# Kernel optimization log

Measured on AMD Instinct MI355X. Metric: run time of the kernel, lower is better.

The kernel has to match this reference:

```python
import jax, jax.numpy as jnp
import numpy as np

V, P = 50000, 50
WE, PE = 300, 100
LH = 800            # bidirectional total hidden
H = LH // 2         # per-direction hidden = 400
MH = 1024           # mlp_hidden_dim
B, T = 32, 128


def setup_inputs() -> dict:
    key = jax.random.key(0)
    ks = jax.random.split(key, 16)
    s = 0.05
    inp = {
        "word_tensor": jax.random.randint(ks[0], (B, T), 0, V, dtype=jnp.int32),
        "word_lengths": jnp.full((B,), T, dtype=jnp.int32),
        "pos_tensor": jax.random.randint(ks[1], (B, T), 0, P, dtype=jnp.int32),
        "word_emb": jax.random.normal(ks[2], (V, WE), jnp.float32) * s,
        "pos_emb": jax.random.normal(ks[3], (P, PE), jnp.float32) * s,
        # LSTM layer 0: input dim WE+PE=400; stacked over 2 directions
        "Wih0": jax.random.normal(ks[4], (2, 4 * H, WE + PE), jnp.float32) * s,
        "Whh0": jax.random.normal(ks[5], (2, 4 * H, H), jnp.float32) * s,
        "b0": jnp.zeros((2, 4 * H), jnp.float32),
        # LSTM layer 1: input dim = 2*H = 800
        "Wih1": jax.random.normal(ks[6], (2, 4 * H, LH), jnp.float32) * s,
        "Whh1": jax.random.normal(ks[7], (2, 4 * H, H), jnp.float32) * s,
        "b1": jnp.zeros((2, 4 * H), jnp.float32),
        "Wh": jax.random.normal(ks[8], (MH // 2, LH), jnp.float32) * s,
        "bh": jnp.zeros((MH // 2,), jnp.float32),
        "Wm": jax.random.normal(ks[9], (MH // 2, LH), jnp.float32) * s,
        "bm": jnp.zeros((MH // 2,), jnp.float32),
        "Wo": jax.random.normal(ks[10], (1, MH), jnp.float32) * s,
        "bo": jnp.zeros((1,), jnp.float32),
    }
    return inp


def _lstm_dir(x_tbd, W_ih, W_hh, bias, reverse):
    # x_tbd: [T,B,D]; PyTorch gate order i,f,g,o
    Bsz = x_tbd.shape[1]
    Hd = W_hh.shape[1]
    def cell(carry, xt):
        h, c = carry
        g = xt @ W_ih.T + h @ W_hh.T + bias
        i, f, gg, o = jnp.split(g, 4, axis=-1)
        c = jax.nn.sigmoid(f) * c + jax.nn.sigmoid(i) * jnp.tanh(gg)
        h = jax.nn.sigmoid(o) * jnp.tanh(c)
        return (h, c), h
    init = (jnp.zeros((Bsz, Hd), x_tbd.dtype), jnp.zeros((Bsz, Hd), x_tbd.dtype))
    _, hs = jax.lax.scan(cell, init, x_tbd, reverse=reverse)
    return hs  # [T,B,H], in original time order


def _bilstm_layer(x_btd, Wih, Whh, b):
    x_tbd = jnp.swapaxes(x_btd, 0, 1)
    fwd = _lstm_dir(x_tbd, Wih[0], Whh[0], b[0], reverse=False)
    bwd = _lstm_dir(x_tbd, Wih[1], Whh[1], b[1], reverse=True)
    out = jnp.concatenate([fwd, bwd], axis=-1)  # [T,B,2H]
    return jnp.swapaxes(out, 0, 1)              # [B,T,2H]


def reference(word_tensor, word_lengths, pos_tensor, word_emb, pos_emb,
              Wih0, Whh0, b0, Wih1, Whh1, b1,
              Wh, bh, Wm, bm, Wo, bo):
    embeds = jnp.concatenate([word_emb[word_tensor], pos_emb[pos_tensor]], axis=2)  # [B,T,400]
    h1 = _bilstm_layer(embeds, Wih0, Whh0, b0)   # [B,T,800]
    lstm_out = _bilstm_layer(h1, Wih1, Whh1, b1)  # [B,T,800]
    head_f = lstm_out @ Wh.T + bh   # [B,T,512]
    modif_f = lstm_out @ Wm.T + bm  # [B,T,512]
    # score[b,h,m] = Wo @ tanh(cat(head_f[b,h], modif_f[b,m])) + bo
    # tanh(cat(a,b)) = cat(tanh(a), tanh(b)) -> exact decomposition
    half = Wo.shape[1] // 2
    s_h = jnp.tanh(head_f) @ Wo[0, :half]   # [B,T]
    s_m = jnp.tanh(modif_f) @ Wo[0, half:]  # [B,T]
    score = s_h[:, :, None] + s_m[:, None, :] + bo[0]  # [B,T,T]
    return score
```

## Files before the change

### kernel.cpp

```cpp
#include <hip/hip_runtime.h>

#define DEV __device__ __forceinline__

typedef _Float16 f16;
typedef _Float16 f16x8 __attribute__((ext_vector_type(8)));
typedef float f32x4 __attribute__((ext_vector_type(4)));
typedef unsigned long long ull;

static constexpr int K0P  = 416;
static constexpr int NBLK = 13;
static constexpr int GN   = 3328;
static constexpr int WKP  = 424;
static constexpr int HX_OFF = 128 * WKP * 2;
static constexpr int FL_OFF = HX_OFF + 13 * 2560;
static constexpr int SMEM_LSTM = FL_OFF + 16;
static constexpr int HB1_ELEM  = 2 * 128 * 13 * 1024;
static constexpr int HB_BYTES  = 2 * HB1_ELEM * 2;
static constexpr unsigned READY0 = 0x80008000u;

DEV float sigf(float x) { return 1.f / (1.f + __expf(-x)); }
DEV float tanhf_(float x) {
  x = fminf(10.f, fmaxf(-10.f, x));
  float e = __expf(2.f * x);
  return (e - 1.f) / (e + 1.f);
}
DEV ull  AL8(const ull* p) { return __hip_atomic_load(p, __ATOMIC_RELAXED, __HIP_MEMORY_SCOPE_AGENT); }
DEV void AS4(unsigned* p, unsigned v) { __hip_atomic_store(p, v, __ATOMIC_RELAXED, __HIP_MEMORY_SCOPE_AGENT); }


__global__ void embed_k(const int* __restrict__ wt, const int* __restrict__ pt,
                        const float* __restrict__ we, const float* __restrict__ pe,
                        f16* __restrict__ x0)
{
  const int r = blockIdx.x;
  const int tid = threadIdx.x;
  const int w = wt[r], p = pt[r];
  const float* wrow = we + (size_t)w * 300;
  const float* prow = pe + (size_t)p * 100;
  f16* xr = x0 + (size_t)r * K0P;
  for (int k = tid; k < K0P; k += 128) {
    float v = (k < 300) ? wrow[k] : (k < 400 ? prow[k - 300] : 0.f);
    xr[k] = (f16)v;
  }
}

__global__ void convpad_k(const float* __restrict__ src, f16* __restrict__ dst,
                          int rows, int K, int KP)
{
  const size_t total = (size_t)rows * KP;
  for (size_t i = (size_t)blockIdx.x * blockDim.x + threadIdx.x; i < total;
       i += (size_t)gridDim.x * blockDim.x) {
    int r = (int)(i / KP), k = (int)(i % KP);
    dst[i] = (f16)(k < K ? src[(size_t)r * K + k] : 0.f);
  }
}

__global__ void wih_reorder_k(const float* __restrict__ src, const float* __restrict__ bias,
                              f16* __restrict__ dst, float* __restrict__ biasr,
                              int K, int KP)
{
  const size_t total = (size_t)GN * KP;
  for (size_t i = (size_t)blockIdx.x * blockDim.x + threadIdx.x; i < total;
       i += (size_t)gridDim.x * blockDim.x) {
    int k = (int)(i % KP);
    int R = (int)(i / KP);
    int d = R / 1664, rr = R % 1664, blk = rr >> 7, loc = rr & 127;
    int w = loc >> 5, t = (loc >> 4) & 1, fq = (loc >> 2) & 3, g = loc & 3;
    int u = blk * 32 + w * 8 + 2 * fq + t;
    float v = (u < 400 && k < K) ? src[((size_t)d * 1600 + g * 400 + u) * K + k] : 0.f;
    dst[i] = (f16)v;
    if (k == 0) biasr[R] = (u < 400) ? bias[d * 1600 + g * 400 + u] : 0.f;
  }
}

__global__ void whh_reorder_k(const float* __restrict__ src, f16* __restrict__ dst)
{
  const int total = 2 * NBLK * 128 * WKP;
  for (int i = blockIdx.x * blockDim.x + threadIdx.x; i < total;
       i += gridDim.x * blockDim.x) {
    int k = i % WKP, loc = (i / WKP) & 127, blk = (i / (WKP * 128)) % NBLK,
        d = i / (WKP * 128 * NBLK);
    int w = loc >> 5, t = (loc >> 4) & 1, fq = (loc >> 2) & 3, g = loc & 3;
    int u = blk * 32 + w * 8 + 2 * fq + t;
    float v = (u < 400 && k < 400) ? src[((size_t)d * 1600 + g * 400 + u) * 400 + k] : 0.f;
    dst[i] = (f16)v;
  }
}

__global__ void biascat_k(const float* __restrict__ bh, const float* __restrict__ bm,
                          float* __restrict__ bhm)
{
  int i = threadIdx.x;
  bhm[i] = i < 512 ? bh[i] : bm[i - 512];
}

__global__ void init_hb_k(unsigned* __restrict__ p, int n)
{
  for (int i = blockIdx.x * blockDim.x + threadIdx.x; i < n; i += gridDim.x * blockDim.x) {
    int off = i % (13 * 512);
    int blk = off >> 9, win = off & 511;
    bool pad = (blk == 12) && ((win >> 7) & 1);
    p[i] = pad ? READY0 : 0u;
  }
}

__global__ __launch_bounds__(256) void gemm_f16_nt(
    const f16* __restrict__ A, const f16* __restrict__ Bw,
    const float* __restrict__ bias, float* __restrict__ C,
    int M, int N, int KP)
{
  __shared__ __align__(16) f16 As[128][40];
  __shared__ __align__(16) f16 Bs[128][40];
  const int tid = threadIdx.x;
  const int bn = blockIdx.x, bm = blockIdx.y;
  const int lane = tid & 63, wid = tid >> 6;
  const int wr = wid >> 1, wc = wid & 1;
  const int srow = tid >> 1, shalf = tid & 1;
  const f16* Ap = A + (size_t)(bm * 128 + srow) * KP + shalf * 16;
  const f16* Bp = Bw + (size_t)(bn * 128 + srow) * KP + shalf * 16;
  const int fr = lane & 15, fq = lane >> 4;
  f32x4 acc[4][4] = {};
  for (int kt = 0; kt < KP; kt += 32) {
    __syncthreads();
    *(uint4*)&As[srow][shalf * 16]     = *(const uint4*)(Ap + kt);
    *(uint4*)&As[srow][shalf * 16 + 8] = *(const uint4*)(Ap + kt + 8);
    *(uint4*)&Bs[srow][shalf * 16]     = *(const uint4*)(Bp + kt);
    *(uint4*)&Bs[srow][shalf * 16 + 8] = *(const uint4*)(Bp + kt + 8);
    __syncthreads();
    f16x8 af[4], bf[4];
    #pragma unroll
    for (int m = 0; m < 4; ++m) af[m] = *(const f16x8*)&As[wr * 64 + m * 16 + fr][fq * 8];
    #pragma unroll
    for (int n = 0; n < 4; ++n) bf[n] = *(const f16x8*)&Bs[wc * 64 + n * 16 + fr][fq * 8];
    #pragma unroll
    for (int m = 0; m < 4; ++m)
      #pragma unroll
      for (int n = 0; n < 4; ++n)
        acc[m][n] = __builtin_amdgcn_mfma_f32_16x16x32_f16(af[m], bf[n], acc[m][n], 0, 0, 0);
  }
  #pragma unroll
  for (int n = 0; n < 4; ++n) {
    const int gn = bn * 128 + wc * 64 + n * 16 + fr;
    const float bv = bias ? bias[gn] : 0.f;
    #pragma unroll
    for (int m = 0; m < 4; ++m) {
      const size_t gm = (size_t)bm * 128 + wr * 64 + m * 16 + fq * 4;
      #pragma unroll
      for (int r = 0; r < 4; ++r)
        C[(gm + r) * (size_t)N + gn] = acc[m][n][r] + bv;
    }
  }
}

__global__ __launch_bounds__(256) void lstm_mfma_k(
    const float* __restrict__ gates,
    const f16* __restrict__ whh_r,
    f16* __restrict__ h_out,
    f16* __restrict__ hB)
{
  extern __shared__ __align__(16) char smem[];
  f16*  W_lds = (f16*)smem;
  char* hx    = smem + HX_OFF;
  int*  flags = (int*)(smem + FL_OFF);

  const int d = blockIdx.x / NBLK, blk = blockIdx.x % NBLK;
  const int tid = threadIdx.x;
  const int lane = tid & 63, w = tid >> 6;
  const int fr = lane & 15, fq = lane >> 4;

  {
    const uint4* src = (const uint4*)(whh_r + ((size_t)d * NBLK + blk) * 128 * WKP);
    uint4* dst = (uint4*)W_lds;
    for (int i = tid; i < 128 * WKP / 8; i += 256) dst[i] = src[i];
  }
  if (tid < 2) flags[tid] = 0;
  __syncthreads();

  const int u0 = blk * 32 + w * 8 + 2 * fq;
  const bool ok = u0 < 400;
  const float* gbase0 = gates + (size_t)(fr * 128) * GN + d * 1664 + blk * 128 + w * 32;
  const float* gbase1 = gbase0 + (size_t)16 * 128 * GN;
  f16* hout0 = h_out + (size_t)(fr * 128) * 800 + d * 400;
  f16* hout1 = hout0 + (size_t)16 * 128 * 800;
  const f16* a0base = W_lds + (size_t)(w * 32 + fr) * WKP + fq * 8;
  const f16* a1base = a0base + 16 * WKP;
  f16* hb_d = hB + (size_t)d * 128 * 13 * 1024;

  const int nkk = (w == 0) ? 4 : 3;
  const int kk0 = (w == 0) ? 0 : 4 + 3 * (w - 1);

  float c00 = 0.f, c01 = 0.f, c10 = 0.f, c11 = 0.f;

  for (int s = 0; s < 128; ++s) {
    const int t = d ? 127 - s : s;
    f32x4 acc00 = {}, acc01 = {}, acc10 = {}, acc11 = {};
    float4 p00, p10, p01, p11;

    if (s > 0) {
      const ull* slab = (const ull*)(hb_d + (size_t)(s - 1) * 13 * 1024) + lane * 2;
      ull q[4][4];
      const unsigned full = (1u << nkk) - 1;
      unsigned pend = (nkk == 4) ? 0xFFFFu : 0x0FFFu;
      unsigned wrote = 0, flagged = 0;
      int* fw = &flags[s & 1];
      while (flagged != full) {
        #pragma unroll
        for (int i = 0; i < 4; ++i)
          if (i < nkk) {
            const ull* pp = slab + (kk0 + i) * 256;
            if ((pend >> (i * 4 + 0)) & 1) q[i][0] = AL8(pp);
            if ((pend >> (i * 4 + 1)) & 1) q[i][1] = AL8(pp + 1);
            if ((pend >> (i * 4 + 2)) & 1) q[i][2] = AL8(pp + 128);
            if ((pend >> (i * 4 + 3)) & 1) q[i][3] = AL8(pp + 129);
          }
        __builtin_amdgcn_sched_barrier(0);
        #pragma unroll
        for (int i = 0; i < 4; ++i)
          if (i < nkk)
            #pragma unroll
            for (int j = 0; j < 4; ++j)
              if ((pend >> (i * 4 + j)) & 1) {
                ull v = q[i][j];
                if ((unsigned)v != 0u && (unsigned)(v >> 32) != 0u)
                  pend &= ~(1u << (i * 4 + j));
              }
        #pragma unroll
        for (int i = 0; i < 4; ++i)
          if (i < nkk && !((wrote >> i) & 1) && ((pend >> (i * 4)) & 15u) == 0u) {
            char* hp = hx + (kk0 + i) * 2560 + lane * 40;
            *(ull*)(hp +  0) = q[i][0];
            *(ull*)(hp +  8) = q[i][1];
            *(ull*)(hp + 16) = q[i][2];
            *(ull*)(hp + 24) = q[i][3];
            wrote |= 1u << i;
          }
        #pragma unroll
        for (int i = 0; i < 4; ++i)
          if (i < nkk && !((flagged >> i) & 1)) {
            bool done = ((pend >> (i * 4)) & 15u) == 0u;
            if (__all(done)) {
              asm volatile("s_waitcnt lgkmcnt(0)" ::: "memory");
              if (lane == 0)
                __hip_atomic_fetch_or(fw, 1 << (kk0 + i), __ATOMIC_RELAXED,
                                      __HIP_MEMORY_SCOPE_WORKGROUP);
              flagged |= 1u << i;
            }
          }
        if (flagged != full) __builtin_amdgcn_s_sleep(2);
      }
      const float* g0 = gbase0 + (size_t)t * GN;
      const float* g1 = gbase1 + (size_t)t * GN;
      p00 = *(const float4*)(g0 + fq * 4);
      p10 = *(const float4*)(g0 + 16 + fq * 4);
      p01 = *(const float4*)(g1 + fq * 4);
      p11 = *(const float4*)(g1 + 16 + fq * 4);
      while ((__hip_atomic_load(fw, __ATOMIC_ACQUIRE, __HIP_MEMORY_SCOPE_WORKGROUP)
              & 0x1FFF) != 0x1FFF)
        __builtin_amdgcn_s_sleep(1);
      __builtin_amdgcn_sched_barrier(0);
      #pragma unroll
      for (int kk = 0; kk < 13; ++kk) {
        const char* hp = hx + kk * 2560 + lane * 40;
        f16x8 a0 = *(const f16x8*)(a0base + kk * 32);
        f16x8 a1 = *(const f16x8*)(a1base + kk * 32);
        union { ull u[2]; f16x8 v; } B0, B1;
        B0.u[0] = *(const ull*)(hp);      B0.u[1] = *(const ull*)(hp + 8);
        B1.u[0] = *(const ull*)(hp + 16); B1.u[1] = *(const ull*)(hp + 24);
        acc00 = __builtin_amdgcn_mfma_f32_16x16x32_f16(a0, B0.v, acc00, 0, 0, 0);
        acc01 = __builtin_amdgcn_mfma_f32_16x16x32_f16(a0, B1.v, acc01, 0, 0, 0);
        acc10 = __builtin_amdgcn_mfma_f32_16x16x32_f16(a1, B0.v, acc10, 0, 0, 0);
        acc11 = __builtin_amdgcn_mfma_f32_16x16x32_f16(a1, B1.v, acc11, 0, 0, 0);
      }
    } else {
      const float* g0 = gbase0 + (size_t)t * GN;
      const float* g1 = gbase1 + (size_t)t * GN;
      p00 = *(const float4*)(g0 + fq * 4);
      p10 = *(const float4*)(g0 + 16 + fq * 4);
      p01 = *(const float4*)(g1 + fq * 4);
      p11 = *(const float4*)(g1 + 16 + fq * 4);
    }

    __syncthreads();
    if (tid == 0)
      __hip_atomic_store(&flags[s & 1], 0, __ATOMIC_RELAXED, __HIP_MEMORY_SCOPE_WORKGROUP);

    auto act = [&](const f32x4& a, const float4& p, float& c) -> f16 {
      float vi = a[0] + p.x, vf = a[1] + p.y, vg = a[2] + p.z, vo = a[3] + p.w;
      c = sigf(vf) * c + sigf(vi) * tanhf_(vg);
      return (f16)(sigf(vo) * tanhf_(c));
    };
    f16 h00 = act(acc00, p00, c00);
    f16 h10 = act(acc10, p10, c10);
    f16 h01 = act(acc01, p01, c01);
    f16 h11 = act(acc11, p11, c11);

    if (ok) {
      unsigned pk0 = (unsigned)__builtin_bit_cast(unsigned short, h00) |
                     ((unsigned)__builtin_bit_cast(unsigned short, h10) << 16);
      unsigned pk1 = (unsigned)__builtin_bit_cast(unsigned short, h01) |
                     ((unsigned)__builtin_bit_cast(unsigned short, h11) << 16);
      if (pk0 == 0u) pk0 = READY0;
      if (pk1 == 0u) pk1 = READY0;
      unsigned* hbw = (unsigned*)(hb_d + (size_t)s * 13 * 1024 + blk * 1024
                                  + (w * 16 + fr) * 8) + fq;
      AS4(hbw, pk0);
      AS4(hbw + 256, pk1);
      *(unsigned*)(hout0 + (size_t)t * 800 + u0) = pk0;
      *(unsigned*)(hout1 + (size_t)t * 800 + u0) = pk1;
    }
  }
}

__global__ __launch_bounds__(256) void tail_k(const float* __restrict__ feat,
                                              const float* __restrict__ wo,
                                              float* __restrict__ s_h,
                                              float* __restrict__ s_m)
{
  const int r = blockIdx.x;
  const int tid = threadIdx.x;
  const float* fr = feat + (size_t)r * 1024;
  float sum = 0.f;
  const int n0 = tid * 4;
  #pragma unroll
  for (int j = 0; j < 4; ++j) sum += tanhf_(fr[n0 + j]) * wo[n0 + j];
  #pragma unroll
  for (int off = 32; off > 0; off >>= 1) sum += __shfl_down(sum, off, 64);
  __shared__ float red[4];
  if ((tid & 63) == 0) red[tid >> 6] = sum;
  __syncthreads();
  if (tid == 0)       s_h[r] = red[0] + red[1];
  else if (tid == 64) s_m[r] = red[2] + red[3];
}

__global__ void score_k(const float* __restrict__ s_h, const float* __restrict__ s_m,
                        const float* __restrict__ bo, float* __restrict__ out)
{
  const int bh = blockIdx.x;
  const int m = threadIdx.x;
  out[(size_t)bh * 128 + m] = s_h[bh] + s_m[(bh & ~127) + m] + bo[0];
}

extern "C" void kernel_launch(void* const* d_in, const int* in_sizes, int n_in,
                              void* d_out, int out_size, void* d_ws, size_t ws_size,
                              hipStream_t stream)
{
  const int*   wt   = (const int*)d_in[0];
  const int*   pt   = (const int*)d_in[2];
  const float* we   = (const float*)d_in[3];
  const float* pe   = (const float*)d_in[4];
  const float* Wih0 = (const float*)d_in[5];
  const float* Whh0 = (const float*)d_in[6];
  const float* b0   = (const float*)d_in[7];
  const float* Wih1 = (const float*)d_in[8];
  const float* Whh1 = (const float*)d_in[9];
  const float* b1   = (const float*)d_in[10];
  const float* Wh   = (const float*)d_in[11];
  const float* bh   = (const float*)d_in[12];
  const float* Wm   = (const float*)d_in[13];
  const float* bm   = (const float*)d_in[14];
  const float* Wo   = (const float*)d_in[15];
  const float* bo   = (const float*)d_in[16];
  float* out = (float*)d_out;

  char* p = (char*)d_ws;
  auto alloc = [&](size_t bytes) { char* q = p; p += (bytes + 255) & ~(size_t)255; return q; };
  f16*   x0    = (f16*)alloc((size_t)4096 * K0P * 2);
  f16*   wihr0 = (f16*)alloc((size_t)GN * K0P * 2);
  f16*   wihr1 = (f16*)alloc((size_t)GN * 800 * 2);
  f16*   whhr0 = (f16*)alloc((size_t)2 * NBLK * 128 * WKP * 2);
  f16*   whhr1 = (f16*)alloc((size_t)2 * NBLK * 128 * WKP * 2);
  f16*   whm   = (f16*)alloc((size_t)1024 * 800 * 2);
  float* biasr0= (float*)alloc(GN * 4);
  float* biasr1= (float*)alloc(GN * 4);
  float* bhm   = (float*)alloc(1024 * 4);
  float* sh    = (float*)alloc(4096 * 4);
  float* sm    = (float*)alloc(4096 * 4);
  f16*   h1    = (f16*)alloc((size_t)4096 * 800 * 2);
  f16*   h2    = (f16*)alloc((size_t)4096 * 800 * 2);
  f16*   hB    = (f16*)alloc(HB_BYTES);
  float* gates = (float*)alloc((size_t)4096 * GN * 4);
  float* feat  = (float*)gates;

  static bool attr_set = false;
  if (!attr_set) {
    hipFuncSetAttribute((const void*)lstm_mfma_k,
                        hipFuncAttributeMaxDynamicSharedMemorySize, SMEM_LSTM);
    attr_set = true;
  }

  init_hb_k<<<512, 256, 0, stream>>>((unsigned*)hB, HB_BYTES / 4);
  embed_k<<<4096, 128, 0, stream>>>(wt, pt, we, pe, x0);
  wih_reorder_k<<<1024, 256, 0, stream>>>(Wih0, b0, wihr0, biasr0, 400, K0P);
  wih_reorder_k<<<1024, 256, 0, stream>>>(Wih1, b1, wihr1, biasr1, 800, 800);
  whh_reorder_k<<<1024, 256, 0, stream>>>(Whh0, whhr0);
  whh_reorder_k<<<1024, 256, 0, stream>>>(Whh1, whhr1);
  convpad_k<<<1024, 256, 0, stream>>>(Wh, whm, 512, 800, 800);
  convpad_k<<<1024, 256, 0, stream>>>(Wm, whm + (size_t)512 * 800, 512, 800, 800);
  biascat_k<<<1, 1024, 0, stream>>>(bh, bm, bhm);

  gemm_f16_nt<<<dim3(26, 32), 256, 0, stream>>>(x0, wihr0, biasr0, gates, 4096, GN, K0P);
  lstm_mfma_k<<<26, 256, SMEM_LSTM, stream>>>(gates, whhr0, h1, hB);
  gemm_f16_nt<<<dim3(26, 32), 256, 0, stream>>>(h1, wihr1, biasr1, gates, 4096, GN, 800);
  lstm_mfma_k<<<26, 256, SMEM_LSTM, stream>>>(gates, whhr1, h2, hB + HB1_ELEM);
  gemm_f16_nt<<<dim3(8, 32), 256, 0, stream>>>(h2, whm, bhm, feat, 4096, 1024, 800);
  tail_k<<<4096, 256, 0, stream>>>(feat, Wo, sh, sm);
  score_k<<<4096, 128, 0, stream>>>(sh, sm, bo, out);
}
```

Measured before the change: 1.366 ms.

## Co-locate each LSTM direction's blocks on one XCD and use non-atomic polling

The recurrent LSTM kernel now launches 256 blocks. Each block reads its XCC id and claims a role so that the 13 blocks of each direction land on the same XCD; extra blocks exit. A probe checks whether all blocks of a direction can see each other's writes through plain volatile accesses; if so, the step-to-step h exchange uses volatile loads and stores instead of agent-scope atomics. The loop also prefetches the next step's input gates and spins with less sleep, and the h_out writes are moved to a separate unpack kernel. This relies on undocumented XCD placement and L2 coherence behaviour, adds launch and handshake overhead, and falls back to the atomic path when the probe fails.

```diff
diff --git a/kernel.cpp b/kernel.cpp
--- a/kernel.cpp
+++ b/kernel.cpp
@@ -26,6 +26,8 @@
 }
 DEV ull  AL8(const ull* p) { return __hip_atomic_load(p, __ATOMIC_RELAXED, __HIP_MEMORY_SCOPE_AGENT); }
 DEV void AS4(unsigned* p, unsigned v) { __hip_atomic_store(p, v, __ATOMIC_RELAXED, __HIP_MEMORY_SCOPE_AGENT); }
+DEV int  ALi(const int* p) { return __hip_atomic_load(p, __ATOMIC_RELAXED, __HIP_MEMORY_SCOPE_AGENT); }
+DEV void AAi(int* p, int v) { __hip_atomic_fetch_add(p, v, __ATOMIC_RELAXED, __HIP_MEMORY_SCOPE_AGENT); }
 
 
 __global__ void embed_k(const int* __restrict__ wt, const int* __restrict__ pt,
@@ -94,6 +96,12 @@
   bhm[i] = i < 512 ? bh[i] : bm[i - 512];
 }
 
+__global__ void zero_k(int* __restrict__ p, int n)
+{
+  for (int i = blockIdx.x * blockDim.x + threadIdx.x; i < n; i += gridDim.x * blockDim.x)
+    p[i] = 0;
+}
+
 __global__ void init_hb_k(unsigned* __restrict__ p, int n)
 {
   for (int i = blockIdx.x * blockDim.x + threadIdx.x; i < n; i += gridDim.x * blockDim.x) {
@@ -101,6 +109,23 @@
     int blk = off >> 9, win = off & 511;
     bool pad = (blk == 12) && ((win >> 7) & 1);
     p[i] = pad ? READY0 : 0u;
+  }
+}
+
+__global__ __launch_bounds__(256) void unpack_k(const f16* __restrict__ hBl,
+                                                f16* __restrict__ h_out)
+{
+  const int d = blockIdx.x >> 7, s = blockIdx.x & 127;
+  const int t = d ? 127 - s : s;
+  const unsigned* slab = (const unsigned*)(hBl + ((size_t)d * 128 + s) * 13 * 1024);
+  for (int j = threadIdx.x; j < 13 * 512; j += 256) {
+    const int blk = j >> 9, q = j & 511, half = q >> 8, q2 = q & 255;
+    const int fq = q2 & 3, fr = (q2 >> 2) & 15, w = q2 >> 6;
+    const int u0 = blk * 32 + w * 8 + 2 * fq;
+    if (u0 < 400) {
+      const int b = fr + 16 * half;
+      *(unsigned*)(h_out + (size_t)(b * 128 + t) * 800 + d * 400 + u0) = slab[j];
+    }
   }
 }
 
@@ -152,66 +177,46 @@
   }
 }
 
-__global__ __launch_bounds__(256) void lstm_mfma_k(
-    const float* __restrict__ gates,
-    const f16* __restrict__ whh_r,
-    f16* __restrict__ h_out,
-    f16* __restrict__ hB)
-{
-  extern __shared__ __align__(16) char smem[];
-  f16*  W_lds = (f16*)smem;
-  char* hx    = smem + HX_OFF;
-  int*  flags = (int*)(smem + FL_OFF);
-
-  const int d = blockIdx.x / NBLK, blk = blockIdx.x % NBLK;
-  const int tid = threadIdx.x;
-  const int lane = tid & 63, w = tid >> 6;
-  const int fr = lane & 15, fq = lane >> 4;
-
-  {
-    const uint4* src = (const uint4*)(whh_r + ((size_t)d * NBLK + blk) * 128 * WKP);
-    uint4* dst = (uint4*)W_lds;
-    for (int i = tid; i < 128 * WKP / 8; i += 256) dst[i] = src[i];
-  }
-  if (tid < 2) flags[tid] = 0;
-  __syncthreads();
-
-  const int u0 = blk * 32 + w * 8 + 2 * fq;
-  const bool ok = u0 < 400;
-  const float* gbase0 = gates + (size_t)(fr * 128) * GN + d * 1664 + blk * 128 + w * 32;
-  const float* gbase1 = gbase0 + (size_t)16 * 128 * GN;
-  f16* hout0 = h_out + (size_t)(fr * 128) * 800 + d * 400;
-  f16* hout1 = hout0 + (size_t)16 * 128 * 800;
-  const f16* a0base = W_lds + (size_t)(w * 32 + fr) * WKP + fq * 8;
-  const f16* a1base = a0base + 16 * WKP;
-  f16* hb_d = hB + (size_t)d * 128 * 13 * 1024;
-
+template<bool FAST>
+DEV void lstm_loop(const float* gbase0, const float* gbase1,
+                   const f16* a0base, const f16* a1base,
+                   f16* hb_d, char* hx, int* lflag,
+                   int d, int blk, int w, int lane, int fr, int fq, int tid, bool ok)
+{
   const int nkk = (w == 0) ? 4 : 3;
   const int kk0 = (w == 0) ? 0 : 4 + 3 * (w - 1);
-
   float c00 = 0.f, c01 = 0.f, c10 = 0.f, c11 = 0.f;
 
+  float4 pc00, pc10, pc01, pc11;
+  {
+    const int t0 = d ? 127 : 0;
+    const float* g0 = gbase0 + (size_t)t0 * GN;
+    const float* g1 = gbase1 + (size_t)t0 * GN;
+    pc00 = *(const float4*)(g0 + fq * 4);
+    pc10 = *(const float4*)(g0 + 16 + fq * 4);
+    pc01 = *(const float4*)(g1 + fq * 4);
+    pc11 = *(const float4*)(g1 + 16 + fq * 4);
+  }
+
   for (int s = 0; s < 128; ++s) {
-    const int t = d ? 127 - s : s;
     f32x4 acc00 = {}, acc01 = {}, acc10 = {}, acc11 = {};
-    float4 p00, p10, p01, p11;
-
+    int* fw = &lflag[s & 1];
     if (s > 0) {
       const ull* slab = (const ull*)(hb_d + (size_t)(s - 1) * 13 * 1024) + lane * 2;
       ull q[4][4];
       const unsigned full = (1u << nkk) - 1;
       unsigned pend = (nkk == 4) ? 0xFFFFu : 0x0FFFu;
       unsigned wrote = 0, flagged = 0;
-      int* fw = &flags[s & 1];
+      int rnd = 0;
       while (flagged != full) {
         #pragma unroll
         for (int i = 0; i < 4; ++i)
           if (i < nkk) {
             const ull* pp = slab + (kk0 + i) * 256;
-            if ((pend >> (i * 4 + 0)) & 1) q[i][0] = AL8(pp);
-            if ((pend >> (i * 4 + 1)) & 1) q[i][1] = AL8(pp + 1);
-            if ((pend >> (i * 4 + 2)) & 1) q[i][2] = AL8(pp + 128);
-            if ((pend >> (i * 4 + 3)) & 1) q[i][3] = AL8(pp + 129);
+            if ((pend >> (i * 4 + 0)) & 1) q[i][0] = FAST ? *(volatile const ull*)pp        : AL8(pp);
+            if ((pend >> (i * 4 + 1)) & 1) q[i][1] = FAST ? *(volatile const ull*)(pp + 1)  : AL8(pp + 1);
+            if ((pend >> (i * 4 + 2)) & 1) q[i][2] = FAST ? *(volatile const ull*)(pp + 128): AL8(pp + 128);
+            if ((pend >> (i * 4 + 3)) & 1) q[i][3] = FAST ? *(volatile const ull*)(pp + 129): AL8(pp + 129);
           }
         __builtin_amdgcn_sched_barrier(0);
         #pragma unroll
@@ -246,14 +251,22 @@
               flagged |= 1u << i;
             }
           }
-        if (flagged != full) __builtin_amdgcn_s_sleep(2);
+        if (flagged != full && ++rnd >= 2) __builtin_amdgcn_s_sleep(1);
       }
-      const float* g0 = gbase0 + (size_t)t * GN;
-      const float* g1 = gbase1 + (size_t)t * GN;
-      p00 = *(const float4*)(g0 + fq * 4);
-      p10 = *(const float4*)(g0 + 16 + fq * 4);
-      p01 = *(const float4*)(g1 + fq * 4);
-      p11 = *(const float4*)(g1 + 16 + fq * 4);
+    }
+
+    float4 pn00 = pc00, pn10 = pc10, pn01 = pc01, pn11 = pc11;
+    if (s < 127) {
+      const int tn = d ? 126 - s : s + 1;
+      const float* g0 = gbase0 + (size_t)tn * GN;
+      const float* g1 = gbase1 + (size_t)tn * GN;
+      pn00 = *(const float4*)(g0 + fq * 4);
+      pn10 = *(const float4*)(g0 + 16 + fq * 4);
+      pn01 = *(const float4*)(g1 + fq * 4);
+      pn11 = *(const float4*)(g1 + 16 + fq * 4);
+    }
+
+    if (s > 0) {
       while ((__hip_atomic_load(fw, __ATOMIC_ACQUIRE, __HIP_MEMORY_SCOPE_WORKGROUP)
               & 0x1FFF) != 0x1FFF)
         __builtin_amdgcn_s_sleep(1);
@@ -271,28 +284,21 @@
         acc10 = __builtin_amdgcn_mfma_f32_16x16x32_f16(a1, B0.v, acc10, 0, 0, 0);
         acc11 = __builtin_amdgcn_mfma_f32_16x16x32_f16(a1, B1.v, acc11, 0, 0, 0);
       }
-    } else {
-      const float* g0 = gbase0 + (size_t)t * GN;
-      const float* g1 = gbase1 + (size_t)t * GN;
-      p00 = *(const float4*)(g0 + fq * 4);
-      p10 = *(const float4*)(g0 + 16 + fq * 4);
-      p01 = *(const float4*)(g1 + fq * 4);
-      p11 = *(const float4*)(g1 + 16 + fq * 4);
     }
 
     __syncthreads();
     if (tid == 0)
-      __hip_atomic_store(&flags[s & 1], 0, __ATOMIC_RELAXED, __HIP_MEMORY_SCOPE_WORKGROUP);
+      __hip_atomic_store(fw, 0, __ATOMIC_RELAXED, __HIP_MEMORY_SCOPE_WORKGROUP);
 
     auto act = [&](const f32x4& a, const float4& p, float& c) -> f16 {
       float vi = a[0] + p.x, vf = a[1] + p.y, vg = a[2] + p.z, vo = a[3] + p.w;
       c = sigf(vf) * c + sigf(vi) * tanhf_(vg);
       return (f16)(sigf(vo) * tanhf_(c));
     };
-    f16 h00 = act(acc00, p00, c00);
-    f16 h10 = act(acc10, p10, c10);
-    f16 h01 = act(acc01, p01, c01);
-    f16 h11 = act(acc11, p11, c11);
+    f16 h00 = act(acc00, pc00, c00);
+    f16 h10 = act(acc10, pc10, c10);
+    f16 h01 = act(acc01, pc01, c01);
+    f16 h11 = act(acc11, pc11, c11);
 
     if (ok) {
       unsigned pk0 = (unsigned)__builtin_bit_cast(unsigned short, h00) |
@@ -303,12 +309,107 @@
       if (pk1 == 0u) pk1 = READY0;
       unsigned* hbw = (unsigned*)(hb_d + (size_t)s * 13 * 1024 + blk * 1024
                                   + (w * 16 + fr) * 8) + fq;
-      AS4(hbw, pk0);
-      AS4(hbw + 256, pk1);
-      *(unsigned*)(hout0 + (size_t)t * 800 + u0) = pk0;
-      *(unsigned*)(hout1 + (size_t)t * 800 + u0) = pk1;
-    }
-  }
+      if (FAST) {
+        *(volatile unsigned*)hbw = pk0;
+        *(volatile unsigned*)(hbw + 256) = pk1;
+      } else {
+        AS4(hbw, pk0);
+        AS4(hbw + 256, pk1);
+      }
+    }
+    pc00 = pn00; pc10 = pn10; pc01 = pn01; pc11 = pn11;
+  }
+}
+
+__global__ __launch_bounds__(256) void lstm_mfma_k(
+    const float* __restrict__ gates,
+    const f16* __restrict__ whh_r,
+    f16* __restrict__ hB,
+    int* __restrict__ ctrl,
+    ull* __restrict__ prb)
+{
+  extern __shared__ __align__(16) char smem[];
+  f16*  W_lds = (f16*)smem;
+  char* hx    = smem + HX_OFF;
+  int*  lflag = (int*)(smem + FL_OFF);
+  __shared__ int role_sh, fast_sh;
+
+  const int tid = threadIdx.x;
+  const int lane = tid & 63, w = tid >> 6;
+  const int fr = lane & 15, fq = lane >> 4;
+
+  if (tid == 0) {
+    int xcc;
+    asm volatile("s_getreg_b32 %0, hwreg(HW_REG_XCC_ID)" : "=s"(xcc));
+    xcc &= 7;
+    int role = -1;
+    if (xcc < 2) {
+      int r = atomicAdd(&ctrl[xcc], 1);
+      if (r < NBLK) role = xcc * NBLK + r;
+    }
+    AAi(&ctrl[2], 1);
+    if (role < 0) {
+      while (ALi(&ctrl[2]) < (int)gridDim.x) __builtin_amdgcn_s_sleep(8);
+      for (int dd = 0; dd < 2 && role < 0; ++dd) {
+        int r = atomicAdd(&ctrl[dd], 1);
+        if (r < NBLK) role = dd * NBLK + r;
+      }
+    }
+    role_sh = (role < 0) ? -1 : (role | ((xcc == role / NBLK) ? 256 : 0));
+  }
+  __syncthreads();
+  const int rs = role_sh;
+  if (rs < 0) return;
+  const int role = rs & 255;
+  const bool home = (rs & 256) != 0;
+  const int d = role / NBLK, blk = role % NBLK;
+
+  {
+    const uint4* src = (const uint4*)(whh_r + ((size_t)d * NBLK + blk) * 128 * WKP);
+    uint4* dst = (uint4*)W_lds;
+    for (int i = tid; i < 128 * WKP / 8; i += 256) dst[i] = src[i];
+  }
+  if (tid < 2) lflag[tid] = 0;
+  __syncthreads();
+
+  if (w == 0) {
+    volatile ull* pb = (volatile ull*)(prb + (size_t)d * 13 * 8);
+    ull sink = (lane < 13) ? pb[lane * 8] : 0;
+    asm volatile("" :: "v"((unsigned)(sink & 1)));
+    if (lane == 0) {
+      AAi(&ctrl[4 + d], 1);
+      while (ALi(&ctrl[4 + d]) < NBLK) __builtin_amdgcn_s_sleep(2);
+      pb[blk * 8] = 0xDEADBEEFCAFEF00Dull;
+    }
+    int seen = 0;
+    for (int r = 0; r < 2048 && !seen; ++r) {
+      ull v = (lane < 13) ? pb[lane * 8] : 1;
+      seen = (~__ballot(v != 0)) == 0ull ? 1 : 0;
+    }
+    if (lane == 0) {
+      AAi(&ctrl[6 + d], (seen && home) ? 1 : 0);
+      AAi(&ctrl[8 + d], 1);
+      while (ALi(&ctrl[8 + d]) < NBLK) __builtin_amdgcn_s_sleep(2);
+      fast_sh = (ALi(&ctrl[6 + d]) == NBLK) ? 1 : 0;
+    }
+  }
+  __syncthreads();
+  const bool fast = fast_sh != 0;
+
+  const int u0 = blk * 32 + w * 8 + 2 * fq;
+  const bool ok = u0 < 400;
+  const float* gbase0 = gates + (size_t)(fr * 128) * GN + d * 1664 + blk * 128 + w * 32;
+  const float* gbase1 = gbase0 + (size_t)16 * 128 * GN;
+  const f16* a0base = W_lds + (size_t)(w * 32 + fr) * WKP + fq * 8;
+  const f16* a1base = a0base + 16 * WKP;
+  f16* hb_d = hB + (size_t)d * 128 * 13 * 1024;
+
+  if (fast)
+    lstm_loop<true >(gbase0, gbase1, a0base, a1base, hb_d, hx, lflag,
+                     d, blk, w, lane, fr, fq, tid, ok);
+  else
+    lstm_loop<false>(gbase0, gbase1, a0base, a1base, hb_d, hx, lflag,
+                     d, blk, w, lane, fr, fq, tid, ok);
 }
 
 __global__ __launch_bounds__(256) void tail_k(const float* __restrict__ feat,
@@ -378,6 +479,8 @@
   f16*   h1    = (f16*)alloc((size_t)4096 * 800 * 2);
   f16*   h2    = (f16*)alloc((size_t)4096 * 800 * 2);
   f16*   hB    = (f16*)alloc(HB_BYTES);
+  int*   ctrl  = (int*)alloc(2 * 16 * 4);
+  ull*   prb   = (ull*)alloc(2 * 208 * 8);
   float* gates = (float*)alloc((size_t)4096 * GN * 4);
   float* feat  = (float*)gates;
 
@@ -389,6 +492,8 @@
   }
 
   init_hb_k<<<512, 256, 0, stream>>>((unsigned*)hB, HB_BYTES / 4);
+  zero_k<<<1, 256, 0, stream>>>(ctrl, 32);
+  zero_k<<<2, 256, 0, stream>>>((int*)prb, 832);
   embed_k<<<4096, 128, 0, stream>>>(wt, pt, we, pe, x0);
   wih_reorder_k<<<1024, 256, 0, stream>>>(Wih0, b0, wihr0, biasr0, 400, K0P);
   wih_reorder_k<<<1024, 256, 0, stream>>>(Wih1, b1, wihr1, biasr1, 800, 800);
@@ -399,9 +504,12 @@
   biascat_k<<<1, 1024, 0, stream>>>(bh, bm, bhm);
 
   gemm_f16_nt<<<dim3(26, 32), 256, 0, stream>>>(x0, wihr0, biasr0, gates, 4096, GN, K0P);
-  lstm_mfma_k<<<26, 256, SMEM_LSTM, stream>>>(gates, whhr0, h1, hB);
+  lstm_mfma_k<<<256, 256, SMEM_LSTM, stream>>>(gates, whhr0, hB, ctrl, prb);
+  unpack_k<<<256, 256, 0, stream>>>(hB, h1);
   gemm_f16_nt<<<dim3(26, 32), 256, 0, stream>>>(h1, wihr1, biasr1, gates, 4096, GN, 800);
-  lstm_mfma_k<<<26, 256, SMEM_LSTM, stream>>>(gates, whhr1, h2, hB + HB1_ELEM);
+  lstm_mfma_k<<<256, 256, SMEM_LSTM, stream>>>(gates, whhr1, hB + HB1_ELEM,
+                                               ctrl + 16, prb + 208);
+  unpack_k<<<256, 256, 0, stream>>>(hB + HB1_ELEM, h2);
   gemm_f16_nt<<<dim3(8, 32), 256, 0, stream>>>(h2, whm, bhm, feat, 4096, 1024, 800);
   tail_k<<<4096, 256, 0, stream>>>(feat, Wo, sh, sm);
   score_k<<<4096, 128, 0, stream>>>(sh, sm, bo, out);
```

Measured after the change: 1.795 ms. 1.31x slower.

## Keep W_hh in registers and overlap recurrent MFMA with per-slice h arrival

Applied to the files above, without the earlier changes.

The recurrent LSTM kernel now holds its W_hh slice in VGPRs instead of LDS. It double-buffers the staged hidden state and replaces the single bitmask barrier with per-slice step counters, so each wave runs MFMAs on K-slices as soon as they arrive rather than waiting for all 13. Gate preactivations for the next step are prefetched, and the strided h_out stores are removed from the serial loop, with a separate unpack kernel scattering the hB buffer into the layer output afterwards. The aim is to shorten the per-timestep critical path in the latency-bound recurrence, at the cost of heavy register pressure (104 extra VGPRs for weights) and two extra kernel launches.

```diff
diff --git a/kernel.cpp b/kernel.cpp
--- a/kernel.cpp
+++ b/kernel.cpp
@@ -11,9 +11,8 @@
 static constexpr int NBLK = 13;
 static constexpr int GN   = 3328;
 static constexpr int WKP  = 424;
-static constexpr int HX_OFF = 128 * WKP * 2;
-static constexpr int FL_OFF = HX_OFF + 13 * 2560;
-static constexpr int SMEM_LSTM = FL_OFF + 16;
+static constexpr int HXP  = 13 * 2560;
+static constexpr int SMEM_LSTM = 2 * HXP + 64;
 static constexpr int HB1_ELEM  = 2 * 128 * 13 * 1024;
 static constexpr int HB_BYTES  = 2 * HB1_ELEM * 2;
 static constexpr unsigned READY0 = 0x80008000u;
@@ -100,7 +99,24 @@
     int off = i % (13 * 512);
     int blk = off >> 9, win = off & 511;
     bool pad = (blk == 12) && ((win >> 7) & 1);
-    p[i] = pad ? READY0 : 0u;
+    AS4(p + i, pad ? READY0 : 0u);
+  }
+}
+
+__global__ __launch_bounds__(256) void unpack_k(const f16* __restrict__ hBl,
+                                                f16* __restrict__ h_out)
+{
+  const int d = blockIdx.x >> 7, s = blockIdx.x & 127;
+  const int t = d ? 127 - s : s;
+  const unsigned* slab = (const unsigned*)(hBl + ((size_t)d * 128 + s) * 13 * 1024);
+  for (int j = threadIdx.x; j < 13 * 512; j += 256) {
+    const int blk = j >> 9, q = j & 511, half = q >> 8, q2 = q & 255;
+    const int fq = q2 & 3, fr = (q2 >> 2) & 15, w = q2 >> 6;
+    const int u0 = blk * 32 + w * 8 + 2 * fq;
+    if (u0 < 400) {
+      const int b = fr + 16 * half;
+      *(unsigned*)(h_out + (size_t)(b * 128 + t) * 800 + d * 400 + u0) = slab[j];
+    }
   }
 }
 
@@ -152,147 +168,155 @@
   }
 }
 
-__global__ __launch_bounds__(256) void lstm_mfma_k(
+__global__ __launch_bounds__(256, 1) void lstm_mfma_k(
     const float* __restrict__ gates,
     const f16* __restrict__ whh_r,
-    f16* __restrict__ h_out,
     f16* __restrict__ hB)
 {
   extern __shared__ __align__(16) char smem[];
-  f16*  W_lds = (f16*)smem;
-  char* hx    = smem + HX_OFF;
-  int*  flags = (int*)(smem + FL_OFF);
+  char* hx   = smem;
+  int*  flds = (int*)(smem + 2 * HXP);
 
   const int d = blockIdx.x / NBLK, blk = blockIdx.x % NBLK;
   const int tid = threadIdx.x;
   const int lane = tid & 63, w = tid >> 6;
   const int fr = lane & 15, fq = lane >> 4;
 
-  {
-    const uint4* src = (const uint4*)(whh_r + ((size_t)d * NBLK + blk) * 128 * WKP);
-    uint4* dst = (uint4*)W_lds;
-    for (int i = tid; i < 128 * WKP / 8; i += 256) dst[i] = src[i];
-  }
-  if (tid < 2) flags[tid] = 0;
-  __syncthreads();
+  if (tid < 13) flds[tid] = -1;
+
+  const f16* wr0 = whh_r + ((size_t)(d * NBLK + blk) * 128 + w * 32 + fr) * WKP + fq * 8;
+  const f16* wr1 = wr0 + (size_t)16 * WKP;
+  f16x8 a0r[13], a1r[13];
+  #pragma unroll
+  for (int kk = 0; kk < 13; ++kk) {
+    a0r[kk] = *(const f16x8*)(wr0 + kk * 32);
+    a1r[kk] = *(const f16x8*)(wr1 + kk * 32);
+  }
 
   const int u0 = blk * 32 + w * 8 + 2 * fq;
   const bool ok = u0 < 400;
   const float* gbase0 = gates + (size_t)(fr * 128) * GN + d * 1664 + blk * 128 + w * 32;
   const float* gbase1 = gbase0 + (size_t)16 * 128 * GN;
-  f16* hout0 = h_out + (size_t)(fr * 128) * 800 + d * 400;
-  f16* hout1 = hout0 + (size_t)16 * 128 * 800;
-  const f16* a0base = W_lds + (size_t)(w * 32 + fr) * WKP + fq * 8;
-  const f16* a1base = a0base + 16 * WKP;
   f16* hb_d = hB + (size_t)d * 128 * 13 * 1024;
-
   const int nkk = (w == 0) ? 4 : 3;
   const int kk0 = (w == 0) ? 0 : 4 + 3 * (w - 1);
+  const unsigned ownfull = (1u << nkk) - 1;
 
   float c00 = 0.f, c01 = 0.f, c10 = 0.f, c11 = 0.f;
+  float4 pc00, pc10, pc01, pc11;
+  {
+    const int t0 = d ? 127 : 0;
+    const float* g0 = gbase0 + (size_t)t0 * GN;
+    const float* g1 = gbase1 + (size_t)t0 * GN;
+    pc00 = *(const float4*)(g0 + fq * 4);
+    pc10 = *(const float4*)(g0 + 16 + fq * 4);
+    pc01 = *(const float4*)(g1 + fq * 4);
+    pc11 = *(const float4*)(g1 + 16 + fq * 4);
+  }
+  __syncthreads();
 
   for (int s = 0; s < 128; ++s) {
-    const int t = d ? 127 - s : s;
     f32x4 acc00 = {}, acc01 = {}, acc10 = {}, acc11 = {};
-    float4 p00, p10, p01, p11;
-
     if (s > 0) {
       const ull* slab = (const ull*)(hb_d + (size_t)(s - 1) * 13 * 1024) + lane * 2;
+      char* hxw = hx + (s & 1) * HXP;
       ull q[4][4];
-      const unsigned full = (1u << nkk) - 1;
       unsigned pend = (nkk == 4) ? 0xFFFFu : 0x0FFFu;
-      unsigned wrote = 0, flagged = 0;
-      int* fw = &flags[s & 1];
-      while (flagged != full) {
-        #pragma unroll
-        for (int i = 0; i < 4; ++i)
-          if (i < nkk) {
-            const ull* pp = slab + (kk0 + i) * 256;
-            if ((pend >> (i * 4 + 0)) & 1) q[i][0] = AL8(pp);
-            if ((pend >> (i * 4 + 1)) & 1) q[i][1] = AL8(pp + 1);
-            if ((pend >> (i * 4 + 2)) & 1) q[i][2] = AL8(pp + 128);
-            if ((pend >> (i * 4 + 3)) & 1) q[i][3] = AL8(pp + 129);
+      unsigned stagedm = 0;
+      unsigned flagged = 0;
+      unsigned done = 0;
+      while (done != 0x1FFFu) {
+        bool progress = false;
+        if (flagged != ownfull) {
+          #pragma unroll
+          for (int i = 0; i < 4; ++i)
+            if (i < nkk && !((flagged >> i) & 1)) {
+              const ull* pp = slab + (kk0 + i) * 256;
+              if ((pend >> (i * 4 + 0)) & 1) q[i][0] = AL8(pp);
+              if ((pend >> (i * 4 + 1)) & 1) q[i][1] = AL8(pp + 1);
+              if ((pend >> (i * 4 + 2)) & 1) q[i][2] = AL8(pp + 128);
+              if ((pend >> (i * 4 + 3)) & 1) q[i][3] = AL8(pp + 129);
+            }
+          __builtin_amdgcn_sched_barrier(0);
+          #pragma unroll
+          for (int i = 0; i < 4; ++i)
+            if (i < nkk && !((flagged >> i) & 1)) {
+              #pragma unroll
+              for (int j = 0; j < 4; ++j)
+                if ((pend >> (i * 4 + j)) & 1) {
+                  ull v = q[i][j];
+                  if ((unsigned)v != 0u && (unsigned)(v >> 32) != 0u)
+                    pend &= ~(1u << (i * 4 + j));
+                }
+              if (!((stagedm >> i) & 1) && ((pend >> (i * 4)) & 15u) == 0u) {
+                char* hp = hxw + (kk0 + i) * 2560 + lane * 40;
+                *(ull*)(hp +  0) = q[i][0];
+                *(ull*)(hp +  8) = q[i][1];
+                *(ull*)(hp + 16) = q[i][2];
+                *(ull*)(hp + 24) = q[i][3];
+                stagedm |= 1u << i;
+              }
+              bool dn = (stagedm >> i) & 1;
+              if (__all(dn)) {
+                asm volatile("s_waitcnt lgkmcnt(0)" ::: "memory");
+                if (lane == 0)
+                  __hip_atomic_store(&flds[kk0 + i], s, __ATOMIC_RELAXED,
+                                     __HIP_MEMORY_SCOPE_WORKGROUP);
+                flagged |= 1u << i;
+                progress = true;
+              }
+            }
+        }
+        {
+          int fv = (lane < 13)
+                     ? __hip_atomic_load(&flds[lane], __ATOMIC_RELAXED,
+                                         __HIP_MEMORY_SCOPE_WORKGROUP)
+                     : 0x7fffffff;
+          unsigned rdy = (unsigned)__ballot(fv >= s) & 0x1FFFu;
+          unsigned todo = rdy & ~done;
+          if (todo) {
+            progress = true;
+            #pragma unroll
+            for (int kk = 0; kk < 13; ++kk)
+              if ((todo >> kk) & 1) {
+                const char* hp = hxw + kk * 2560 + lane * 40;
+                union { ull u[2]; f16x8 v; } B0, B1;
+                B0.u[0] = *(const ull*)(hp);      B0.u[1] = *(const ull*)(hp + 8);
+                B1.u[0] = *(const ull*)(hp + 16); B1.u[1] = *(const ull*)(hp + 24);
+                acc00 = __builtin_amdgcn_mfma_f32_16x16x32_f16(a0r[kk], B0.v, acc00, 0, 0, 0);
+                acc01 = __builtin_amdgcn_mfma_f32_16x16x32_f16(a0r[kk], B1.v, acc01, 0, 0, 0);
+                acc10 = __builtin_amdgcn_mfma_f32_16x16x32_f16(a1r[kk], B0.v, acc10, 0, 0, 0);
+                acc11 = __builtin_amdgcn_mfma_f32_16x16x32_f16(a1r[kk], B1.v, acc11, 0, 0, 0);
+              }
+            done |= todo;
           }
-        __builtin_amdgcn_sched_barrier(0);
-        #pragma unroll
-        for (int i = 0; i < 4; ++i)
-          if (i < nkk)
-            #pragma unroll
-            for (int j = 0; j < 4; ++j)
-              if ((pend >> (i * 4 + j)) & 1) {
-                ull v = q[i][j];
-                if ((unsigned)v != 0u && (unsigned)(v >> 32) != 0u)
-                  pend &= ~(1u << (i * 4 + j));
-              }
-        #pragma unroll
-        for (int i = 0; i < 4; ++i)
-          if (i < nkk && !((wrote >> i) & 1) && ((pend >> (i * 4)) & 15u) == 0u) {
-            char* hp = hx + (kk0 + i) * 2560 + lane * 40;
-            *(ull*)(hp +  0) = q[i][0];
-            *(ull*)(hp +  8) = q[i][1];
-            *(ull*)(hp + 16) = q[i][2];
-            *(ull*)(hp + 24) = q[i][3];
-            wrote |= 1u << i;
-          }
-        #pragma unroll
-        for (int i = 0; i < 4; ++i)
-          if (i < nkk && !((flagged >> i) & 1)) {
-            bool done = ((pend >> (i * 4)) & 15u) == 0u;
-            if (__all(done)) {
-              asm volatile("s_waitcnt lgkmcnt(0)" ::: "memory");
-              if (lane == 0)
-                __hip_atomic_fetch_or(fw, 1 << (kk0 + i), __ATOMIC_RELAXED,
-                                      __HIP_MEMORY_SCOPE_WORKGROUP);
-              flagged |= 1u << i;
-            }
-          }
-        if (flagged != full) __builtin_amdgcn_s_sleep(2);
+        }
+        if (!progress && done != 0x1FFFu) __builtin_amdgcn_s_sleep(1);
       }
-      const float* g0 = gbase0 + (size_t)t * GN;
-      const float* g1 = gbase1 + (size_t)t * GN;
-      p00 = *(const float4*)(g0 + fq * 4);
-      p10 = *(const float4*)(g0 + 16 + fq * 4);
-      p01 = *(const float4*)(g1 + fq * 4);
-      p11 = *(const float4*)(g1 + 16 + fq * 4);
-      while ((__hip_atomic_load(fw, __ATOMIC_ACQUIRE, __HIP_MEMORY_SCOPE_WORKGROUP)
-              & 0x1FFF) != 0x1FFF)
-        __builtin_amdgcn_s_sleep(1);
-      __builtin_amdgcn_sched_barrier(0);
-      #pragma unroll
-      for (int kk = 0; kk < 13; ++kk) {
-        const char* hp = hx + kk * 2560 + lane * 40;
-        f16x8 a0 = *(const f16x8*)(a0base + kk * 32);
-        f16x8 a1 = *(const f16x8*)(a1base + kk * 32);
-        union { ull u[2]; f16x8 v; } B0, B1;
-        B0.u[0] = *(const ull*)(hp);      B0.u[1] = *(const ull*)(hp + 8);
-        B1.u[0] = *(const ull*)(hp + 16); B1.u[1] = *(const ull*)(hp + 24);
-        acc00 = __builtin_amdgcn_mfma_f32_16x16x32_f16(a0, B0.v, acc00, 0, 0, 0);
-        acc01 = __builtin_amdgcn_mfma_f32_16x16x32_f16(a0, B1.v, acc01, 0, 0, 0);
-        acc10 = __builtin_amdgcn_mfma_f32_16x16x32_f16(a1, B0.v, acc10, 0, 0, 0);
-        acc11 = __builtin_amdgcn_mfma_f32_16x16x32_f16(a1, B1.v, acc11, 0, 0, 0);
-      }
-    } else {
-      const float* g0 = gbase0 + (size_t)t * GN;
-      const float* g1 = gbase1 + (size_t)t * GN;
-      p00 = *(const float4*)(g0 + fq * 4);
-      p10 = *(const float4*)(g0 + 16 + fq * 4);
-      p01 = *(const float4*)(g1 + fq * 4);
-      p11 = *(const float4*)(g1 + 16 + fq * 4);
     }
 
+    float4 pn00 = pc00, pn10 = pc10, pn01 = pc01, pn11 = pc11;
+    if (s < 127) {
+      const int tn = d ? 126 - s : s + 1;
+      const float* g0 = gbase0 + (size_t)tn * GN;
+      const float* g1 = gbase1 + (size_t)tn * GN;
+      pn00 = *(const float4*)(g0 + fq * 4);
+      pn10 = *(const float4*)(g0 + 16 + fq * 4);
+      pn01 = *(const float4*)(g1 + fq * 4);
+      pn11 = *(const float4*)(g1 + 16 + fq * 4);
+    }
+
     __syncthreads();
-    if (tid == 0)
-      __hip_atomic_store(&flags[s & 1], 0, __ATOMIC_RELAXED, __HIP_MEMORY_SCOPE_WORKGROUP);
 
     auto act = [&](const f32x4& a, const float4& p, float& c) -> f16 {
       float vi = a[0] + p.x, vf = a[1] + p.y, vg = a[2] + p.z, vo = a[3] + p.w;
       c = sigf(vf) * c + sigf(vi) * tanhf_(vg);
       return (f16)(sigf(vo) * tanhf_(c));
     };
-    f16 h00 = act(acc00, p00, c00);
-    f16 h10 = act(acc10, p10, c10);
-    f16 h01 = act(acc01, p01, c01);
-    f16 h11 = act(acc11, p11, c11);
+    f16 h00 = act(acc00, pc00, c00);
+    f16 h10 = act(acc10, pc10, c10);
+    f16 h01 = act(acc01, pc01, c01);
+    f16 h11 = act(acc11, pc11, c11);
 
     if (ok) {
       unsigned pk0 = (unsigned)__builtin_bit_cast(unsigned short, h00) |
@@ -305,9 +329,8 @@
                                   + (w * 16 + fr) * 8) + fq;
       AS4(hbw, pk0);
       AS4(hbw + 256, pk1);
-      *(unsigned*)(hout0 + (size_t)t * 800 + u0) = pk0;
-      *(unsigned*)(hout1 + (size_t)t * 800 + u0) = pk1;
     }
+    pc00 = pn00; pc10 = pn10; pc01 = pn01; pc11 = pn11;
   }
 }
 
@@ -399,9 +422,11 @@
   biascat_k<<<1, 1024, 0, stream>>>(bh, bm, bhm);
 
   gemm_f16_nt<<<dim3(26, 32), 256, 0, stream>>>(x0, wihr0, biasr0, gates, 4096, GN, K0P);
-  lstm_mfma_k<<<26, 256, SMEM_LSTM, stream>>>(gates, whhr0, h1, hB);
+  lstm_mfma_k<<<26, 256, SMEM_LSTM, stream>>>(gates, whhr0, hB);
+  unpack_k<<<256, 256, 0, stream>>>(hB, h1);
   gemm_f16_nt<<<dim3(26, 32), 256, 0, stream>>>(h1, wihr1, biasr1, gates, 4096, GN, 800);
-  lstm_mfma_k<<<26, 256, SMEM_LSTM, stream>>>(gates, whhr1, h2, hB + HB1_ELEM);
+  lstm_mfma_k<<<26, 256, SMEM_LSTM, stream>>>(gates, whhr1, hB + HB1_ELEM);
+  unpack_k<<<256, 256, 0, stream>>>(hB + HB1_ELEM, h2);
   gemm_f16_nt<<<dim3(8, 32), 256, 0, stream>>>(h2, whm, bhm, feat, 4096, 1024, 800);
   tail_k<<<4096, 256, 0, stream>>>(feat, Wo, sh, sm);
   score_k<<<4096, 128, 0, stream>>>(sh, sm, bo, out);
```

Measured after the change: 1.624 ms. 1.19x slower.

## Move h output scatter out of recurrent LSTM loop into separate unpack kernel

Applied to the files above, without the earlier changes.

The recurrent LSTM kernel no longer writes each step's hidden state to the [B,T,800] output. It keeps only the exchange-buffer stores, and a new unpack kernel later copies the exchange slabs into the layout the next GEMM reads. This takes strided global stores off the latency-critical serial recurrence. The polling loop also spins three rounds before sleeping, and sleeps for less time. The cost is two extra kernel launches and an extra read of the exchange buffer.

```diff
diff --git a/kernel.cpp b/kernel.cpp
--- a/kernel.cpp
+++ b/kernel.cpp
@@ -101,6 +101,23 @@
     int blk = off >> 9, win = off & 511;
     bool pad = (blk == 12) && ((win >> 7) & 1);
     p[i] = pad ? READY0 : 0u;
+  }
+}
+
+__global__ __launch_bounds__(256) void unpack_k(const f16* __restrict__ hBl,
+                                                f16* __restrict__ h_out)
+{
+  const int d = blockIdx.x >> 7, s = blockIdx.x & 127;
+  const int t = d ? 127 - s : s;
+  const unsigned* slab = (const unsigned*)(hBl + ((size_t)d * 128 + s) * 13 * 1024);
+  for (int j = threadIdx.x; j < 13 * 512; j += 256) {
+    const int blk = j >> 9, q = j & 511, half = q >> 8, q2 = q & 255;
+    const int fq = q2 & 3, fr = (q2 >> 2) & 15, w = q2 >> 6;
+    const int u0 = blk * 32 + w * 8 + 2 * fq;
+    if (u0 < 400) {
+      const int b = fr + 16 * half;
+      *(unsigned*)(h_out + (size_t)(b * 128 + t) * 800 + d * 400 + u0) = slab[j];
+    }
   }
 }
 
@@ -155,7 +172,6 @@
 __global__ __launch_bounds__(256) void lstm_mfma_k(
     const float* __restrict__ gates,
     const f16* __restrict__ whh_r,
-    f16* __restrict__ h_out,
     f16* __restrict__ hB)
 {
   extern __shared__ __align__(16) char smem[];
@@ -180,8 +196,6 @@
   const bool ok = u0 < 400;
   const float* gbase0 = gates + (size_t)(fr * 128) * GN + d * 1664 + blk * 128 + w * 32;
   const float* gbase1 = gbase0 + (size_t)16 * 128 * GN;
-  f16* hout0 = h_out + (size_t)(fr * 128) * 800 + d * 400;
-  f16* hout1 = hout0 + (size_t)16 * 128 * 800;
   const f16* a0base = W_lds + (size_t)(w * 32 + fr) * WKP + fq * 8;
   const f16* a1base = a0base + 16 * WKP;
   f16* hb_d = hB + (size_t)d * 128 * 13 * 1024;
@@ -202,6 +216,7 @@
       const unsigned full = (1u << nkk) - 1;
       unsigned pend = (nkk == 4) ? 0xFFFFu : 0x0FFFu;
       unsigned wrote = 0, flagged = 0;
+      int rnd = 0;
       int* fw = &flags[s & 1];
       while (flagged != full) {
         #pragma unroll
@@ -246,7 +261,7 @@
               flagged |= 1u << i;
             }
           }
-        if (flagged != full) __builtin_amdgcn_s_sleep(2);
+        if (flagged != full && ++rnd >= 3) __builtin_amdgcn_s_sleep(1);
       }
       const float* g0 = gbase0 + (size_t)t * GN;
       const float* g1 = gbase1 + (size_t)t * GN;
@@ -305,8 +320,6 @@
                                   + (w * 16 + fr) * 8) + fq;
       AS4(hbw, pk0);
       AS4(hbw + 256, pk1);
-      *(unsigned*)(hout0 + (size_t)t * 800 + u0) = pk0;
-      *(unsigned*)(hout1 + (size_t)t * 800 + u0) = pk1;
     }
   }
 }
@@ -399,9 +412,11 @@
   biascat_k<<<1, 1024, 0, stream>>>(bh, bm, bhm);
 
   gemm_f16_nt<<<dim3(26, 32), 256, 0, stream>>>(x0, wihr0, biasr0, gates, 4096, GN, K0P);
-  lstm_mfma_k<<<26, 256, SMEM_LSTM, stream>>>(gates, whhr0, h1, hB);
+  lstm_mfma_k<<<26, 256, SMEM_LSTM, stream>>>(gates, whhr0, hB);
+  unpack_k<<<256, 256, 0, stream>>>(hB, h1);
   gemm_f16_nt<<<dim3(26, 32), 256, 0, stream>>>(h1, wihr1, biasr1, gates, 4096, GN, 800);
-  lstm_mfma_k<<<26, 256, SMEM_LSTM, stream>>>(gates, whhr1, h2, hB + HB1_ELEM);
+  lstm_mfma_k<<<26, 256, SMEM_LSTM, stream>>>(gates, whhr1, hB + HB1_ELEM);
+  unpack_k<<<256, 256, 0, stream>>>(hB + HB1_ELEM, h2);
   gemm_f16_nt<<<dim3(8, 32), 256, 0, stream>>>(h2, whm, bhm, feat, 4096, 1024, 800);
   tail_k<<<4096, 256, 0, stream>>>(feat, Wo, sh, sm);
   score_k<<<4096, 128, 0, stream>>>(sh, sm, bo, out);
```

Result: no change. 1.387 ms (+1.6%).
